# Kernel tuning notes

Hardware: AMD Instinct MI355X
Metric: run time of the kernel (lower is better)

## Reference

```python
import jax, jax.numpy as jnp
import numpy as np

B, N, C = 8, 4096, 256
HEADS = 8
DH = C // HEADS
SR = 4
EPS = 1e-5


def setup_inputs() -> dict:
    key = jax.random.key(0)
    ks = jax.random.split(key, 12)
    s = 0.02
    inp = {
        "x": jax.random.normal(ks[0], (B, N, C), dtype=jnp.float32),
        "H": 64,
        "W": 64,
        # nn.Linear weights stored torch-style [out, in]
        "q_w": jax.random.normal(ks[1], (C, C), dtype=jnp.float32) * s,
        "q_b": jax.random.normal(ks[2], (C,), dtype=jnp.float32) * s,
        "kv_w": jax.random.normal(ks[3], (2 * C, C), dtype=jnp.float32) * s,
        "kv_b": jax.random.normal(ks[4], (2 * C,), dtype=jnp.float32) * s,
        # Conv2d weight torch OIHW [C, C, SR, SR]
        "sr_w": jax.random.normal(ks[5], (C, C, SR, SR), dtype=jnp.float32) * s,
        "sr_b": jax.random.normal(ks[6], (C,), dtype=jnp.float32) * s,
        "ln_g": jnp.ones((C,), dtype=jnp.float32),
        "ln_b": jnp.zeros((C,), dtype=jnp.float32),
        "proj_w": jax.random.normal(ks[7], (C, C), dtype=jnp.float32) * s,
        "proj_b": jax.random.normal(ks[8], (C,), dtype=jnp.float32) * s,
    }
    return inp


def _layernorm(x, g, b):
    mu = jnp.mean(x, axis=-1, keepdims=True)
    var = jnp.mean(jnp.square(x - mu), axis=-1, keepdims=True)
    return (x - mu) * jax.lax.rsqrt(var + EPS) * g + b


def reference(x, H, W, q_w, q_b, kv_w, kv_b, sr_w, sr_b, ln_g, ln_b, proj_w, proj_b):
    b, n, c = x.shape
    scale = 1.0 / jnp.sqrt(jnp.float32(DH))

    # q projection -> [b, heads, n, dh]
    q = (x @ q_w.T + q_b).reshape(b, n, HEADS, DH).transpose(0, 2, 1, 3)

    # spatial reduction: conv stride=SR kernel=SR on the [b,H,W,c] image
    x_img = x.reshape(b, H, W, c)  # NHWC
    kern = jnp.transpose(sr_w, (2, 3, 1, 0))  # OIHW -> HWIO
    x_sr = jax.lax.conv_general_dilated(
        x_img, kern, window_strides=(SR, SR), padding="VALID",
        dimension_numbers=("NHWC", "HWIO", "NHWC")) + sr_b
    n_kv = (H // SR) * (W // SR)
    x_sr = x_sr.reshape(b, n_kv, c)
    x_sr = _layernorm(x_sr, ln_g, ln_b)

    # kv projection -> k, v: [b, heads, n_kv, dh]
    kv = (x_sr @ kv_w.T + kv_b).reshape(b, n_kv, 2, HEADS, DH)
    kv = kv.transpose(2, 0, 3, 1, 4)
    k, v = kv[0], kv[1]

    # attention (dropout rates are 0.0 / eval mode)
    attn = jnp.einsum("bhnd,bhmd->bhnm", q, k) * scale
    attn = jax.nn.softmax(attn, axis=-1)
    out = jnp.einsum("bhnm,bhmd->bhnd", attn, v)
    out = out.transpose(0, 2, 1, 3).reshape(b, n, c)
    return out @ proj_w.T + proj_b
```

## Files before the change

kernel.cpp:

```cpp
#include <hip/hip_runtime.h>

typedef unsigned short u16;
typedef float f32x4 __attribute__((ext_vector_type(4)));
typedef __bf16 bf16x4 __attribute__((ext_vector_type(4)));
typedef __bf16 bf16x8 __attribute__((ext_vector_type(8)));

#define B_ 8
#define N_ 4096
#define C_ 256
#define NKV 256
#define CEXP 0.25506604f

__device__ inline u16 f2bf(float f) {
    union { float f; unsigned u; } v; v.f = f;
    unsigned r = v.u + 0x7FFF + ((v.u >> 16) & 1);
    return (u16)(r >> 16);
}

__device__ inline void gload16(const void* g, void* l) {
    __builtin_amdgcn_global_load_lds(
        (const __attribute__((address_space(1))) void*)g,
        (__attribute__((address_space(3))) void*)l, 16, 0, 0);
}

__global__ __launch_bounds__(256) void prep_all(
    const float* __restrict__ x, u16* __restrict__ xb,
    const float* __restrict__ qw, const float* __restrict__ kvw,
    const float* __restrict__ pw, const float* __restrict__ srw,
    u16* __restrict__ wqb, u16* __restrict__ wkv, u16* __restrict__ wp, u16* __restrict__ wsr)
{
    size_t base = ((size_t)blockIdx.x * 256 + threadIdx.x) * 4;
    float4 v = *(const float4*)(x + base);
    ushort4 o;
    o.x = f2bf(v.x); o.y = f2bf(v.y); o.z = f2bf(v.z); o.w = f2bf(v.w);
    *(ushort4*)(xb + base) = o;

    int t = blockIdx.x * 256 + threadIdx.x;
    int stride = gridDim.x * 256;
    for (int i = t; i < 65536; i += stride) { wqb[i] = f2bf(qw[i]); wp[i] = f2bf(pw[i]); }
    for (int i = t; i < 131072; i += stride) wkv[i] = f2bf(kvw[i]);
    for (int i = t; i < 1048576; i += stride) {
        int oo = i >> 12, kk = i & 4095;
        int ci = kk & 255, khkw = kk >> 8;
        wsr[i] = f2bf(srw[(size_t)(oo * 256 + ci) * 16 + khkw]);
    }
}

template<int OUTMODE, bool IM2COL>
__device__ __forceinline__ void gemm_body(
    u16* As, u16* Bs,
    const u16* __restrict__ A, const u16* __restrict__ Bt,
    const float* __restrict__ bias, void* __restrict__ outp,
    int M, int Nn, int K, int kchunk, int bm, int bn, int bz)
{
    const int tid = threadIdx.x;
    const int k0 = bz * kchunk;
    const int wid = tid >> 6, lane = tid & 63;
    const int wr = wid >> 1, wc = wid & 1;
    const int lrow = lane & 15, lkg = lane >> 4;

    f32x4 acc[4][4] = {};

    const u16 *aS[4], *bS[4];
#pragma unroll
    for (int j = 0; j < 4; ++j) {
        const int c = tid + 256 * j;
        const int s = c >> 9, r = (c & 511) >> 2, p2 = c & 3;
        const int colo = s * 32 + p2 * 8;
        if constexpr (IM2COL) {
            const int g = bm * 128 + r;
            const int bb = g >> 8, p = g & 255;
            aS[j] = A + (size_t)(bb * 4096 + (p >> 4) * 256 + (p & 15) * 4) * 256 + colo;
        } else {
            aS[j] = A + (size_t)(bm * 128 + r) * K + k0 + colo;
        }
        bS[j] = Bt + (size_t)(bn * 128 + r) * K + k0 + colo;
    }

    for (int kk = 0; kk < kchunk; kk += 64) {
        int aoff;
        if constexpr (IM2COL) {
            const int K0 = k0 + kk;
            const int khkw = K0 >> 8;
            aoff = ((khkw >> 2) * 64 + (khkw & 3)) * 256 + (K0 & 255);
        } else {
            aoff = kk;
        }
#pragma unroll
        for (int j = 0; j < 4; ++j) {
            gload16(aS[j] + aoff, As + tid * 8 + j * 2048);
            gload16(bS[j] + kk,  Bs + tid * 8 + j * 2048);
        }
        __syncthreads();
#pragma unroll
        for (int ks = 0; ks < 2; ++ks) {
            bf16x8 af[4], bff[4];
#pragma unroll
            for (int i = 0; i < 4; ++i) {
                af[i]  = *(const bf16x8*)(As + ks * 4096 + (wr * 64 + i * 16 + lrow) * 32 + lkg * 8);
                bff[i] = *(const bf16x8*)(Bs + ks * 4096 + (wc * 64 + i * 16 + lrow) * 32 + lkg * 8);
            }
#pragma unroll
            for (int i = 0; i < 4; ++i)
#pragma unroll
                for (int j = 0; j < 4; ++j)
                    acc[i][j] = __builtin_amdgcn_mfma_f32_16x16x32_bf16(af[i], bff[j], acc[i][j], 0, 0, 0);
        }
        __syncthreads();
    }

    const int row0 = bm * 128 + wr * 64;
    const int col0 = bn * 128 + wc * 64;
    if constexpr (OUTMODE == 2) {
        float* o = (float*)outp + (size_t)bz * M * Nn;
#pragma unroll
        for (int i = 0; i < 4; ++i)
#pragma unroll
            for (int j = 0; j < 4; ++j)
#pragma unroll
                for (int reg = 0; reg < 4; ++reg)
                    o[(size_t)(row0 + i * 16 + lkg * 4 + reg) * Nn + col0 + j * 16 + lrow] = acc[i][j][reg];
    } else {
#pragma unroll
        for (int j = 0; j < 4; ++j) {
            const int col = col0 + j * 16 + lrow;
            float bv = bias[col];
#pragma unroll
            for (int i = 0; i < 4; ++i)
#pragma unroll
                for (int reg = 0; reg < 4; ++reg) {
                    const size_t idx = (size_t)(row0 + i * 16 + lkg * 4 + reg) * Nn + col;
                    const float val = acc[i][j][reg] + bv;
                    if constexpr (OUTMODE == 1) ((u16*)outp)[idx] = f2bf(val);
                    else                        ((float*)outp)[idx] = val;
                }
        }
    }
}

template<int OUTMODE, bool IM2COL>
__global__ __launch_bounds__(256, 2) void gemm128(
    const u16* __restrict__ A, const u16* __restrict__ Bt,
    const float* __restrict__ bias, void* __restrict__ outp,
    int M, int Nn, int K, int kchunk)
{
    __shared__ __align__(16) u16 As[128 * 64];
    __shared__ __align__(16) u16 Bs[128 * 64];
    gemm_body<OUTMODE, IM2COL>(As, Bs, A, Bt, bias, outp, M, Nn, K, kchunk,
                               blockIdx.x, blockIdx.y, blockIdx.z);
}

__global__ __launch_bounds__(256, 2) void fused_convq(
    const u16* __restrict__ xb, const u16* __restrict__ wsr, float* __restrict__ part,
    const u16* __restrict__ wqb, const float* __restrict__ qb, u16* __restrict__ qbuf)
{
    __shared__ __align__(16) u16 As[128 * 64];
    __shared__ __align__(16) u16 Bs[128 * 64];
    const int id = blockIdx.x;
    if (id < 256) {
        const int z = id & 7, t = id >> 3;
        gemm_body<2, true>(As, Bs, xb, wsr, nullptr, part,
                           2048, 256, 4096, 512, t >> 1, t & 1, z);
    } else {
        const int qid = id - 256;
        gemm_body<1, false>(As, Bs, xb, wqb, qb, qbuf,
                            32768, 256, 256, 256, qid >> 1, qid & 1, 0);
    }
}

__global__ __launch_bounds__(256) void ln_kernel(
    const float* __restrict__ part, const float* __restrict__ srb,
    const float* __restrict__ g, const float* __restrict__ bb, u16* __restrict__ out)
{
    const int row = blockIdx.x, c = threadIdx.x;
    const size_t idx = (size_t)row * 256 + c;
    float v = srb[c];
#pragma unroll
    for (int z = 0; z < 8; ++z) v += part[idx + (size_t)z * 524288];
    float s = v;
#pragma unroll
    for (int m = 1; m < 64; m <<= 1) s += __shfl_xor(s, m);
    __shared__ float red[4];
    if ((c & 63) == 0) red[c >> 6] = s;
    __syncthreads();
    float tot = red[0] + red[1] + red[2] + red[3];
    float mu = tot * (1.0f / 256.0f);
    float d = v - mu;
    float s2 = d * d;
#pragma unroll
    for (int m = 1; m < 64; m <<= 1) s2 += __shfl_xor(s2, m);
    __syncthreads();
    if ((c & 63) == 0) red[c >> 6] = s2;
    __syncthreads();
    float var = (red[0] + red[1] + red[2] + red[3]) * (1.0f / 256.0f);
    out[idx] = f2bf(d * rsqrtf(var + 1e-5f) * g[c] + bb[c]);
}

__global__ __launch_bounds__(256, 2) void gemm64_kv(
    const u16* __restrict__ A, const u16* __restrict__ Bt,
    const float* __restrict__ bias, u16* __restrict__ outp)
{
    __shared__ __align__(16) u16 As[64 * 32];
    __shared__ __align__(16) u16 Bs[64 * 32];
    const int tid = threadIdx.x, bm = blockIdx.x, bn = blockIdx.y;
    const int wid = tid >> 6, lane = tid & 63;
    const int wr = wid >> 1, wc = wid & 1;
    const int lrow = lane & 15, lkg = lane >> 4;

    f32x4 acc[2][2] = {};
    const int r = tid >> 2, cl = (tid & 3) * 8;
    const u16* aS = A  + (size_t)(bm * 64 + r) * 256 + cl;
    const u16* bS = Bt + (size_t)(bn * 64 + r) * 256 + cl;
    u16* aD = As + tid * 8;
    u16* bD = Bs + tid * 8;

    for (int kk = 0; kk < 256; kk += 32) {
        gload16(aS + kk, aD);
        gload16(bS + kk, bD);
        __syncthreads();
        bf16x8 af[2], bf2[2];
#pragma unroll
        for (int i = 0; i < 2; ++i) {
            af[i]  = *(const bf16x8*)(As + (wr * 32 + i * 16 + lrow) * 32 + lkg * 8);
            bf2[i] = *(const bf16x8*)(Bs + (wc * 32 + i * 16 + lrow) * 32 + lkg * 8);
        }
#pragma unroll
        for (int i = 0; i < 2; ++i)
#pragma unroll
            for (int j = 0; j < 2; ++j)
                acc[i][j] = __builtin_amdgcn_mfma_f32_16x16x32_bf16(af[i], bf2[j], acc[i][j], 0, 0, 0);
        __syncthreads();
    }

    const int row0 = bm * 64 + wr * 32;
    const int col0 = bn * 64 + wc * 32;
#pragma unroll
    for (int j = 0; j < 2; ++j) {
        const int col = col0 + j * 16 + lrow;
        const float bv = bias[col];
        const float sc = (col < 256) ? CEXP : 1.0f;
#pragma unroll
        for (int i = 0; i < 2; ++i)
#pragma unroll
            for (int reg = 0; reg < 4; ++reg)
                outp[(size_t)(row0 + i * 16 + lkg * 4 + reg) * 512 + col] =
                    f2bf((acc[i][j][reg] + bv) * sc);
    }
}

__global__ __launch_bounds__(256, 4) void attn_kernel(
    const u16* __restrict__ qbuf, const u16* __restrict__ kvbuf, u16* __restrict__ obuf)
{
    __shared__ __align__(16) u16 Ks[256 * 32];
    __shared__ __align__(16) u16 Vt[32 * 264];
    const int logical = (blockIdx.x & 7) * 512 + (blockIdx.x >> 3);
    const int b = logical >> 9, h = (logical >> 6) & 7, qt = logical & 63;
    const int tid = threadIdx.x;
    const int wid = tid >> 6, lane = tid & 63;
    const int lrow = lane & 15, lkg = lane >> 4;

    {
        const int loff = (lane * 16) ^ (((lane >> 3) & 7) << 4);
        const int rloc = loff >> 6, piece = (loff >> 4) & 3;
#pragma unroll
        for (int i = 0; i < 4; ++i) {
            const int c = wid * 4 + i;
            const u16* src = kvbuf + (size_t)(b * 256 + c * 16 + rloc) * 512 + h * 32 + piece * 8;
            gload16(src, Ks + c * 512);
        }
    }
    {
        const int i = tid & 127, dbase = (tid >> 7) * 16;
        const u16* vs0 = kvbuf + (size_t)(b * 256 + 2 * i) * 512 + 256 + h * 32 + dbase;
        const u16* vs1 = vs0 + 512;
        ushort4 a0 = *(const ushort4*)(vs0);
        ushort4 a1 = *(const ushort4*)(vs0 + 4);
        ushort4 a2 = *(const ushort4*)(vs0 + 8);
        ushort4 a3 = *(const ushort4*)(vs0 + 12);
        ushort4 b0 = *(const ushort4*)(vs1);
        ushort4 b1 = *(const ushort4*)(vs1 + 4);
        ushort4 b2 = *(const ushort4*)(vs1 + 8);
        ushort4 b3 = *(const ushort4*)(vs1 + 12);
        unsigned* vw = (unsigned*)(Vt + (size_t)dbase * 264 + 2 * i);
#define VPACK(d, lo, hi) vw[(d) * 132] = ((unsigned)(hi) << 16) | (lo)
        VPACK(0,  a0.x, b0.x); VPACK(1,  a0.y, b0.y); VPACK(2,  a0.z, b0.z); VPACK(3,  a0.w, b0.w);
        VPACK(4,  a1.x, b1.x); VPACK(5,  a1.y, b1.y); VPACK(6,  a1.z, b1.z); VPACK(7,  a1.w, b1.w);
        VPACK(8,  a2.x, b2.x); VPACK(9,  a2.y, b2.y); VPACK(10, a2.z, b2.z); VPACK(11, a2.w, b2.w);
        VPACK(12, a3.x, b3.x); VPACK(13, a3.y, b3.y); VPACK(14, a3.z, b3.z); VPACK(15, a3.w, b3.w);
#undef VPACK
    }

    const int qcol = h * 32 + lkg * 8;
    bf16x8 qf = *(const bf16x8*)(qbuf +
        (size_t)(b * 4096 + qt * 64 + wid * 16 + lrow) * 256 + qcol);

    bf16x8 onesf = {};
    if (lrow == 0) {
#pragma unroll
        for (int e = 0; e < 8; ++e) onesf[e] = (__bf16)1.0f;
    }

    __syncthreads();

    const int pbase = (lrow * 64 + lkg * 16) ^ (((lrow >> 1) & 7) << 4);
    f32x4 acc[16];
#pragma unroll
    for (int nf = 0; nf < 16; ++nf) acc[nf] = (f32x4){0.f, 0.f, 0.f, 0.f};
#pragma unroll
    for (int nf = 0; nf < 16; ++nf) {
        bf16x8 kfr = *(const bf16x8*)((const char*)Ks + pbase + nf * 1024);
        acc[nf] = __builtin_amdgcn_mfma_f32_16x16x32_bf16(kfr, qf, acc[nf], 0, 0, 0);
    }

    bf16x8 pa8[8];
#pragma unroll
    for (int nf2 = 0; nf2 < 8; ++nf2) {
        bf16x8 pv;
#pragma unroll
        for (int half = 0; half < 2; ++half) {
#pragma unroll
            for (int r = 0; r < 4; ++r)
                pv[half * 4 + r] = (__bf16)exp2f(acc[2 * nf2 + half][r]);
        }
        pa8[nf2] = pv;
    }

    f32x4 o0 = (f32x4){0.f, 0.f, 0.f, 0.f};
    f32x4 o1 = (f32x4){0.f, 0.f, 0.f, 0.f};
    f32x4 o2 = (f32x4){0.f, 0.f, 0.f, 0.f};
#pragma unroll
    for (int nf2 = 0; nf2 < 8; ++nf2) {
        bf16x4 lo0 = *(const bf16x4*)(Vt + lrow * 264 + nf2 * 32 + lkg * 4);
        bf16x4 hi0 = *(const bf16x4*)(Vt + lrow * 264 + nf2 * 32 + 16 + lkg * 4);
        bf16x4 lo1 = *(const bf16x4*)(Vt + (16 + lrow) * 264 + nf2 * 32 + lkg * 4);
        bf16x4 hi1 = *(const bf16x4*)(Vt + (16 + lrow) * 264 + nf2 * 32 + 16 + lkg * 4);
        bf16x8 v0 = __builtin_shufflevector(lo0, hi0, 0, 1, 2, 3, 4, 5, 6, 7);
        bf16x8 v1 = __builtin_shufflevector(lo1, hi1, 0, 1, 2, 3, 4, 5, 6, 7);
        o0 = __builtin_amdgcn_mfma_f32_16x16x32_bf16(pa8[nf2], v0, o0, 0, 0, 0);
        o1 = __builtin_amdgcn_mfma_f32_16x16x32_bf16(pa8[nf2], v1, o1, 0, 0, 0);
        o2 = __builtin_amdgcn_mfma_f32_16x16x32_bf16(pa8[nf2], onesf, o2, 0, 0, 0);
    }

    float invq[4];
#pragma unroll
    for (int r = 0; r < 4; ++r)
        invq[r] = __shfl(__builtin_amdgcn_rcpf(o2[r]), lane & 48);

    const size_t obase = (size_t)(b * 4096 + qt * 64 + wid * 16);
#pragma unroll
    for (int r = 0; r < 4; ++r) {
        u16* op = obuf + (obase + lkg * 4 + r) * 256 + h * 32 + lrow;
        op[0]  = f2bf(o0[r] * invq[r]);
        op[16] = f2bf(o1[r] * invq[r]);
    }
}

extern "C" void kernel_launch(void* const* d_in, const int* in_sizes, int n_in,
                              void* d_out, int out_size, void* d_ws, size_t ws_size,
                              hipStream_t stream)
{
    (void)in_sizes; (void)n_in; (void)out_size; (void)ws_size;
    const float* x   = (const float*)d_in[0];
    const float* qw  = (const float*)d_in[3];
    const float* qb  = (const float*)d_in[4];
    const float* kvw = (const float*)d_in[5];
    const float* kvb = (const float*)d_in[6];
    const float* srw = (const float*)d_in[7];
    const float* srb = (const float*)d_in[8];
    const float* lng = (const float*)d_in[9];
    const float* lnb = (const float*)d_in[10];
    const float* pw  = (const float*)d_in[11];
    const float* pb  = (const float*)d_in[12];

    char* ws = (char*)d_ws;
    u16*   xb      = (u16*)(ws + 0);
    u16*   att     = (u16*)(ws + 16777216);
    float* part    = (float*)(ws + 33554432);
    u16*   wsr     = (u16*)(ws + 50331648);
    u16*   wqb     = (u16*)(ws + 52428800);
    u16*   wkvb    = (u16*)(ws + 52559872);
    u16*   wpb     = (u16*)(ws + 52822016);
    u16*   xsr     = (u16*)(ws + 52953088);
    u16*   kvo     = (u16*)(ws + 54001664);
    u16*   qbuf    = (u16*)d_out;

    prep_all<<<8192, 256, 0, stream>>>(x, xb, qw, kvw, pw, srw, wqb, wkvb, wpb, wsr);
    fused_convq<<<768, 256, 0, stream>>>(xb, wsr, part, wqb, qb, qbuf);
    ln_kernel<<<2048, 256, 0, stream>>>(part, srb, lng, lnb, xsr);
    gemm64_kv<<<dim3(32, 8), 256, 0, stream>>>(xsr, wkvb, kvb, kvo);
    attn_kernel<<<4096, 256, 0, stream>>>(qbuf, kvo, att);
    gemm128<0, false><<<dim3(256, 2, 1), 256, 0, stream>>>(att, wpb, pb, d_out, 32768, 256, 256, 256);
}
```

Baseline: 84.87 us.

## Process two query tiles per attention block and widen KV GEMM K-step

The attention kernel now handles 128 query rows per block in two sequential 64-row tiles, so each K/V staging into shared memory is reused twice and the grid is halved. This targets redundant global K/V loads and the per-block transpose work. The KV GEMM also loads a 64-wide K slab per iteration, which halves the number of barriers. The trade-offs are fewer blocks in the grid and longer serial work per block.

```diff
diff --git a/kernel.cpp b/kernel.cpp
--- a/kernel.cpp
+++ b/kernel.cpp
@@ -200,35 +200,45 @@
     const u16* __restrict__ A, const u16* __restrict__ Bt,
     const float* __restrict__ bias, u16* __restrict__ outp)
 {
-    __shared__ __align__(16) u16 As[64 * 32];
-    __shared__ __align__(16) u16 Bs[64 * 32];
+    __shared__ __align__(16) u16 As[64 * 64];
+    __shared__ __align__(16) u16 Bs[64 * 64];
     const int tid = threadIdx.x, bm = blockIdx.x, bn = blockIdx.y;
     const int wid = tid >> 6, lane = tid & 63;
     const int wr = wid >> 1, wc = wid & 1;
     const int lrow = lane & 15, lkg = lane >> 4;
 
     f32x4 acc[2][2] = {};
-    const int r = tid >> 2, cl = (tid & 3) * 8;
-    const u16* aS = A  + (size_t)(bm * 64 + r) * 256 + cl;
-    const u16* bS = Bt + (size_t)(bn * 64 + r) * 256 + cl;
-    u16* aD = As + tid * 8;
-    u16* bD = Bs + tid * 8;
-
-    for (int kk = 0; kk < 256; kk += 32) {
-        gload16(aS + kk, aD);
-        gload16(bS + kk, bD);
+    const u16 *aS[2], *bS[2];
+#pragma unroll
+    for (int j = 0; j < 2; ++j) {
+        const int c = tid + 256 * j;
+        const int s = c >> 8, r = (c & 255) >> 2, p2 = c & 3;
+        const int colo = s * 32 + p2 * 8;
+        aS[j] = A  + (size_t)(bm * 64 + r) * 256 + colo;
+        bS[j] = Bt + (size_t)(bn * 64 + r) * 256 + colo;
+    }
+
+    for (int kk = 0; kk < 256; kk += 64) {
+#pragma unroll
+        for (int j = 0; j < 2; ++j) {
+            gload16(aS[j] + kk, As + tid * 8 + j * 2048);
+            gload16(bS[j] + kk, Bs + tid * 8 + j * 2048);
+        }
         __syncthreads();
-        bf16x8 af[2], bf2[2];
-#pragma unroll
-        for (int i = 0; i < 2; ++i) {
-            af[i]  = *(const bf16x8*)(As + (wr * 32 + i * 16 + lrow) * 32 + lkg * 8);
-            bf2[i] = *(const bf16x8*)(Bs + (wc * 32 + i * 16 + lrow) * 32 + lkg * 8);
-        }
-#pragma unroll
-        for (int i = 0; i < 2; ++i)
-#pragma unroll
-            for (int j = 0; j < 2; ++j)
-                acc[i][j] = __builtin_amdgcn_mfma_f32_16x16x32_bf16(af[i], bf2[j], acc[i][j], 0, 0, 0);
+#pragma unroll
+        for (int ks = 0; ks < 2; ++ks) {
+            bf16x8 af[2], bf2[2];
+#pragma unroll
+            for (int i = 0; i < 2; ++i) {
+                af[i]  = *(const bf16x8*)(As + ks * 2048 + (wr * 32 + i * 16 + lrow) * 32 + lkg * 8);
+                bf2[i] = *(const bf16x8*)(Bs + ks * 2048 + (wc * 32 + i * 16 + lrow) * 32 + lkg * 8);
+            }
+#pragma unroll
+            for (int i = 0; i < 2; ++i)
+#pragma unroll
+                for (int j = 0; j < 2; ++j)
+                    acc[i][j] = __builtin_amdgcn_mfma_f32_16x16x32_bf16(af[i], bf2[j], acc[i][j], 0, 0, 0);
+        }
         __syncthreads();
     }
 
@@ -253,8 +263,8 @@
 {
     __shared__ __align__(16) u16 Ks[256 * 32];
     __shared__ __align__(16) u16 Vt[32 * 264];
-    const int logical = (blockIdx.x & 7) * 512 + (blockIdx.x >> 3);
-    const int b = logical >> 9, h = (logical >> 6) & 7, qt = logical & 63;
+    const int logical = (blockIdx.x & 7) * 256 + (blockIdx.x >> 3);
+    const int b = logical >> 8, h = (logical >> 5) & 7, qt2 = logical & 31;
     const int tid = threadIdx.x;
     const int wid = tid >> 6, lane = tid & 63;
     const int lrow = lane & 15, lkg = lane >> 4;
@@ -291,8 +301,8 @@
     }
 
     const int qcol = h * 32 + lkg * 8;
-    bf16x8 qf = *(const bf16x8*)(qbuf +
-        (size_t)(b * 4096 + qt * 64 + wid * 16 + lrow) * 256 + qcol);
+    const u16* qrow = qbuf + (size_t)(b * 4096 + qt2 * 128 + wid * 16 + lrow) * 256 + qcol;
+    bf16x8 qfA = *(const bf16x8*)(qrow);
 
     bf16x8 onesf = {};
     if (lrow == 0) {
@@ -303,56 +313,62 @@
     __syncthreads();
 
     const int pbase = (lrow * 64 + lkg * 16) ^ (((lrow >> 1) & 7) << 4);
-    f32x4 acc[16];
-#pragma unroll
-    for (int nf = 0; nf < 16; ++nf) acc[nf] = (f32x4){0.f, 0.f, 0.f, 0.f};
-#pragma unroll
-    for (int nf = 0; nf < 16; ++nf) {
-        bf16x8 kfr = *(const bf16x8*)((const char*)Ks + pbase + nf * 1024);
-        acc[nf] = __builtin_amdgcn_mfma_f32_16x16x32_bf16(kfr, qf, acc[nf], 0, 0, 0);
-    }
-
-    bf16x8 pa8[8];
-#pragma unroll
-    for (int nf2 = 0; nf2 < 8; ++nf2) {
-        bf16x8 pv;
-#pragma unroll
-        for (int half = 0; half < 2; ++half) {
-#pragma unroll
-            for (int r = 0; r < 4; ++r)
-                pv[half * 4 + r] = (__bf16)exp2f(acc[2 * nf2 + half][r]);
-        }
-        pa8[nf2] = pv;
-    }
-
-    f32x4 o0 = (f32x4){0.f, 0.f, 0.f, 0.f};
-    f32x4 o1 = (f32x4){0.f, 0.f, 0.f, 0.f};
-    f32x4 o2 = (f32x4){0.f, 0.f, 0.f, 0.f};
-#pragma unroll
-    for (int nf2 = 0; nf2 < 8; ++nf2) {
-        bf16x4 lo0 = *(const bf16x4*)(Vt + lrow * 264 + nf2 * 32 + lkg * 4);
-        bf16x4 hi0 = *(const bf16x4*)(Vt + lrow * 264 + nf2 * 32 + 16 + lkg * 4);
-        bf16x4 lo1 = *(const bf16x4*)(Vt + (16 + lrow) * 264 + nf2 * 32 + lkg * 4);
-        bf16x4 hi1 = *(const bf16x4*)(Vt + (16 + lrow) * 264 + nf2 * 32 + 16 + lkg * 4);
-        bf16x8 v0 = __builtin_shufflevector(lo0, hi0, 0, 1, 2, 3, 4, 5, 6, 7);
-        bf16x8 v1 = __builtin_shufflevector(lo1, hi1, 0, 1, 2, 3, 4, 5, 6, 7);
-        o0 = __builtin_amdgcn_mfma_f32_16x16x32_bf16(pa8[nf2], v0, o0, 0, 0, 0);
-        o1 = __builtin_amdgcn_mfma_f32_16x16x32_bf16(pa8[nf2], v1, o1, 0, 0, 0);
-        o2 = __builtin_amdgcn_mfma_f32_16x16x32_bf16(pa8[nf2], onesf, o2, 0, 0, 0);
-    }
-
-    float invq[4];
-#pragma unroll
-    for (int r = 0; r < 4; ++r)
-        invq[r] = __shfl(__builtin_amdgcn_rcpf(o2[r]), lane & 48);
-
-    const size_t obase = (size_t)(b * 4096 + qt * 64 + wid * 16);
-#pragma unroll
-    for (int r = 0; r < 4; ++r) {
-        u16* op = obuf + (obase + lkg * 4 + r) * 256 + h * 32 + lrow;
-        op[0]  = f2bf(o0[r] * invq[r]);
-        op[16] = f2bf(o1[r] * invq[r]);
-    }
+
+#define ATTN_TILE(TI, QF)                                                               \
+    {                                                                                   \
+        f32x4 acc[16];                                                                  \
+        _Pragma("unroll")                                                               \
+        for (int nf = 0; nf < 16; ++nf) acc[nf] = (f32x4){0.f, 0.f, 0.f, 0.f};          \
+        _Pragma("unroll")                                                               \
+        for (int nf = 0; nf < 16; ++nf) {                                               \
+            bf16x8 kfr = *(const bf16x8*)((const char*)Ks + pbase + nf * 1024);         \
+            acc[nf] = __builtin_amdgcn_mfma_f32_16x16x32_bf16(kfr, (QF), acc[nf], 0, 0, 0); \
+        }                                                                               \
+        bf16x8 pa8[8];                                                                  \
+        _Pragma("unroll")                                                               \
+        for (int nf2 = 0; nf2 < 8; ++nf2) {                                             \
+            bf16x8 pv;                                                                  \
+            _Pragma("unroll")                                                           \
+            for (int half = 0; half < 2; ++half) {                                      \
+                _Pragma("unroll")                                                       \
+                for (int r = 0; r < 4; ++r)                                             \
+                    pv[half * 4 + r] = (__bf16)exp2f(acc[2 * nf2 + half][r]);           \
+            }                                                                           \
+            pa8[nf2] = pv;                                                              \
+        }                                                                               \
+        f32x4 o0 = (f32x4){0.f, 0.f, 0.f, 0.f};                                         \
+        f32x4 o1 = (f32x4){0.f, 0.f, 0.f, 0.f};                                         \
+        f32x4 o2 = (f32x4){0.f, 0.f, 0.f, 0.f};                                         \
+        _Pragma("unroll")                                                               \
+        for (int nf2 = 0; nf2 < 8; ++nf2) {                                             \
+            bf16x4 lo0 = *(const bf16x4*)(Vt + lrow * 264 + nf2 * 32 + lkg * 4);        \
+            bf16x4 hi0 = *(const bf16x4*)(Vt + lrow * 264 + nf2 * 32 + 16 + lkg * 4);   \
+            bf16x4 lo1 = *(const bf16x4*)(Vt + (16 + lrow) * 264 + nf2 * 32 + lkg * 4); \
+            bf16x4 hi1 = *(const bf16x4*)(Vt + (16 + lrow) * 264 + nf2 * 32 + 16 + lkg * 4); \
+            bf16x8 v0 = __builtin_shufflevector(lo0, hi0, 0, 1, 2, 3, 4, 5, 6, 7);      \
+            bf16x8 v1 = __builtin_shufflevector(lo1, hi1, 0, 1, 2, 3, 4, 5, 6, 7);      \
+            o0 = __builtin_amdgcn_mfma_f32_16x16x32_bf16(pa8[nf2], v0, o0, 0, 0, 0);    \
+            o1 = __builtin_amdgcn_mfma_f32_16x16x32_bf16(pa8[nf2], v1, o1, 0, 0, 0);    \
+            o2 = __builtin_amdgcn_mfma_f32_16x16x32_bf16(pa8[nf2], onesf, o2, 0, 0, 0); \
+        }                                                                               \
+        float invq[4];                                                                  \
+        _Pragma("unroll")                                                               \
+        for (int r = 0; r < 4; ++r)                                                     \
+            invq[r] = __shfl(__builtin_amdgcn_rcpf(o2[r]), lane & 48);                  \
+        const size_t obase = (size_t)(b * 4096 + qt2 * 128 + (TI) * 64 + wid * 16);     \
+        _Pragma("unroll")                                                               \
+        for (int r = 0; r < 4; ++r) {                                                   \
+            u16* op = obuf + (obase + lkg * 4 + r) * 256 + h * 32 + lrow;               \
+            op[0]  = f2bf(o0[r] * invq[r]);                                             \
+            op[16] = f2bf(o1[r] * invq[r]);                                             \
+        }                                                                               \
+    }
+
+    ATTN_TILE(0, qfA)
+    __builtin_amdgcn_sched_barrier(0);
+    bf16x8 qfB = *(const bf16x8*)(qrow + 64 * 256);
+    ATTN_TILE(1, qfB)
+#undef ATTN_TILE
 }
 
 extern "C" void kernel_launch(void* const* d_in, const int* in_sizes, int n_in,
@@ -388,6 +404,6 @@
     fused_convq<<<768, 256, 0, stream>>>(xb, wsr, part, wqb, qb, qbuf);
     ln_kernel<<<2048, 256, 0, stream>>>(part, srb, lng, lnb, xsr);
     gemm64_kv<<<dim3(32, 8), 256, 0, stream>>>(xsr, wkvb, kvb, kvo);
-    attn_kernel<<<4096, 256, 0, stream>>>(qbuf, kvo, att);
+    attn_kernel<<<2048, 256, 0, stream>>>(qbuf, kvo, att);
     gemm128<0, false><<<dim3(256, 2, 1), 256, 0, stream>>>(att, wpb, pb, d_out, 32768, 256, 256, 256);
 }
```

New measurement: 83.94 us. No clear change (-1.1%).
